# Optimization experiments

Measured on AMD Instinct MI355X. Metric: run time of the kernel, lower is better.

## Reference

```python
import jax, jax.numpy as jnp
import numpy as np

USER_NUM = 100000
ITEM_NUM = 100000
EMB = 128
N_USERS = 65536
N_BEH = 2097152
N_GROUPS = 2048


def setup_inputs() -> dict:
    key = jax.random.key(0)
    ks = jax.random.split(key, 7)
    user_ids = jax.random.randint(ks[0], (N_USERS,), 0, USER_NUM, dtype=jnp.int32)
    user_group_ids = jnp.sort(jax.random.randint(ks[1], (N_USERS,), 0, N_GROUPS, dtype=jnp.int32))
    behavior_item_ids = jax.random.randint(ks[2], (N_BEH,), 0, ITEM_NUM, dtype=jnp.int32)
    behavior_counts = jax.random.uniform(ks[3], (N_BEH,), dtype=jnp.float32)
    behavior_user_ids = jnp.sort(jax.random.randint(ks[4], (N_BEH,), 0, N_USERS, dtype=jnp.int32))
    user_table = jax.random.normal(ks[5], (USER_NUM, EMB), dtype=jnp.float32)
    item_table = jax.random.normal(ks[6], (ITEM_NUM, EMB), dtype=jnp.float32)
    return {
        "user_ids": user_ids,
        "user_group_ids": user_group_ids,
        "behavior_item_ids": behavior_item_ids,
        "behavior_counts": behavior_counts,
        "behavior_user_ids": behavior_user_ids,
        "user_table": user_table,
        "item_table": item_table,
        "num_groups": N_GROUPS,
    }


def reference(user_ids, user_group_ids, behavior_item_ids, behavior_counts,
              behavior_user_ids, user_table, item_table, num_groups):
    n_users = user_ids.shape[0]
    # weighted bag-of-items per user: sum_j item_emb[b_id] * count  -> [n_users, EMB]
    beh_emb = item_table[behavior_item_ids] * behavior_counts[:, None]
    per_user_beh = jax.ops.segment_sum(beh_emb, behavior_user_ids, num_segments=n_users)
    # user embedding with padding_idx=0 (id 0 -> zero vector)
    ue = user_table[user_ids] * (user_ids != 0).astype(user_table.dtype)[:, None]
    per_user = per_user_beh * ue  # personalized behavior embedding
    # pooling == 'sum' over users within each group -> [num_groups, EMB]
    group_embedding = jax.ops.segment_sum(per_user, user_group_ids, num_segments=num_groups)
    return group_embedding
```

## Files before the change

kernel.cpp:

```cpp
#include <hip/hip_runtime.h>
#include <hip/hip_fp16.h>

#define EMB 128

__global__ __launch_bounds__(256) void convert_kernel(
    const float* __restrict__ src, __half* __restrict__ dst, int n8)
{
    int t = blockIdx.x * 256 + threadIdx.x;
    if (t >= n8) return;
    const float4* s = (const float4*)src + (size_t)t * 2;
    float4 f0 = s[0];
    float4 f1 = s[1];
    union { __half h[8]; uint4 u; } pk;
    pk.h[0] = __float2half_rn(f0.x); pk.h[1] = __float2half_rn(f0.y);
    pk.h[2] = __float2half_rn(f0.z); pk.h[3] = __float2half_rn(f0.w);
    pk.h[4] = __float2half_rn(f1.x); pk.h[5] = __float2half_rn(f1.y);
    pk.h[6] = __float2half_rn(f1.z); pk.h[7] = __float2half_rn(f1.w);
    ((uint4*)dst)[t] = pk.u;
}

__global__ __launch_bounds__(256) void boundary_kernel(
    const int* __restrict__ beh_user, int* __restrict__ start,
    int n_beh, int n_users)
{
    int j = blockIdx.x * 256 + threadIdx.x;
    if (j >= n_beh) return;
    int cur  = beh_user[j];
    int prev = (j == 0) ? -1 : beh_user[j - 1];
    if (cur != prev) {
        for (int u = prev + 1; u <= cur; ++u) start[u] = j;
    }
    if (j == n_beh - 1) {
        for (int u = cur + 1; u <= n_users; ++u) start[u] = n_beh;
    }
}

__global__ __launch_bounds__(256) void per_user_kernel(
    const int*    __restrict__ user_ids,
    const int*    __restrict__ group_ids,
    const int*    __restrict__ beh_item,
    const float*  __restrict__ beh_cnt,
    const int*    __restrict__ beh_user,
    const float*  __restrict__ user_table,
    const __half* __restrict__ item_f16,
    const int*    __restrict__ start,
    float*        __restrict__ out,
    int n_users, int n_beh)
{
    const int lane = threadIdx.x & 63;
    const int half = lane >> 5;
    const int sub  = lane & 31;
    const int wave = threadIdx.x >> 6;
    const int user = blockIdx.x * 4 + wave;

    __shared__ float lds_acc[EMB];
    __shared__ int   lds_grp[4];
    if (threadIdx.x < EMB) lds_acc[threadIdx.x] = 0.0f;

    float4 acc = make_float4(0.f, 0.f, 0.f, 0.f);
    int g = -1;

    if (user < n_users) {
        int s, e;
        if (start) {
            s = start[user];
            e = start[user + 1];
        } else {
            int lo = 0, hi = n_beh;
            while (lo < hi) { int m = (lo + hi) >> 1; if (beh_user[m] < user) lo = m + 1; else hi = m; }
            s = lo;
            hi = n_beh;
            while (lo < hi) { int m = (lo + hi) >> 1; if (beh_user[m] <= user) lo = m + 1; else hi = m; }
            e = lo;
        }

        const __half* itp = item_f16 + sub * 4;

        int j = s;
        for (; j + 16 <= e; j += 16) {
            const int base = j + half * 8;
            int   bidx[8];
            float bcnt[8];
            #pragma unroll
            for (int k = 0; k < 8; ++k) { bidx[k] = beh_item[base + k]; bcnt[k] = beh_cnt[base + k]; }
            uint2 raw[8];
            #pragma unroll
            for (int k = 0; k < 8; ++k)
                raw[k] = *(const uint2*)(itp + (size_t)bidx[k] * EMB);
            #pragma unroll
            for (int k = 0; k < 8; ++k) {
                float2 f01 = __half22float2(*(const __half2*)&raw[k].x);
                float2 f23 = __half22float2(*(const __half2*)&raw[k].y);
                float  c   = bcnt[k];
                acc.x = fmaf(f01.x, c, acc.x);
                acc.y = fmaf(f01.y, c, acc.y);
                acc.z = fmaf(f23.x, c, acc.z);
                acc.w = fmaf(f23.y, c, acc.w);
            }
        }
        for (; j < e; j += 2) {
            int   jj = j + half;
            int   bi = 0;
            float c  = 0.f;
            if (jj < e) { bi = beh_item[jj]; c = beh_cnt[jj]; }
            uint2 raw = *(const uint2*)(itp + (size_t)bi * EMB);
            float2 f01 = __half22float2(*(const __half2*)&raw.x);
            float2 f23 = __half22float2(*(const __half2*)&raw.y);
            acc.x = fmaf(f01.x, c, acc.x);
            acc.y = fmaf(f01.y, c, acc.y);
            acc.z = fmaf(f23.x, c, acc.z);
            acc.w = fmaf(f23.y, c, acc.w);
        }

        acc.x += __shfl_xor(acc.x, 32, 64);
        acc.y += __shfl_xor(acc.y, 32, 64);
        acc.z += __shfl_xor(acc.z, 32, 64);
        acc.w += __shfl_xor(acc.w, 32, 64);

        int uid = user_ids[user];
        float4 ue = make_float4(0.f, 0.f, 0.f, 0.f);
        if (uid != 0) ue = *(const float4*)(user_table + (size_t)uid * EMB + sub * 4);
        acc.x *= ue.x; acc.y *= ue.y; acc.z *= ue.z; acc.w *= ue.w;

        g = group_ids[user];
    }

    const int   d0 = sub * 4 + half * 2;
    const float v0 = half ? acc.z : acc.x;
    const float v1 = half ? acc.w : acc.y;

    if (lane == 0) lds_grp[wave] = g;
    __syncthreads();

    int g0 = lds_grp[0];
    bool same = (g0 >= 0) && (lds_grp[1] == g0) && (lds_grp[2] == g0) && (lds_grp[3] == g0);
    if (same) {
        atomicAdd(&lds_acc[d0],     v0);
        atomicAdd(&lds_acc[d0 + 1], v1);
        __syncthreads();
        if (wave == 0) {
            atomicAdd(&out[(size_t)g0 * EMB + d0],     lds_acc[d0]);
            atomicAdd(&out[(size_t)g0 * EMB + d0 + 1], lds_acc[d0 + 1]);
        }
    } else if (g >= 0) {
        atomicAdd(&out[(size_t)g * EMB + d0],     v0);
        atomicAdd(&out[(size_t)g * EMB + d0 + 1], v1);
    }
}

__global__ __launch_bounds__(256) void per_user_f32_kernel(
    const int*   __restrict__ user_ids,
    const int*   __restrict__ group_ids,
    const int*   __restrict__ beh_item,
    const float* __restrict__ beh_cnt,
    const int*   __restrict__ beh_user,
    const float* __restrict__ user_table,
    const float* __restrict__ item_f32,
    float*       __restrict__ out,
    int n_users, int n_beh)
{
    const int lane = threadIdx.x & 63;
    const int wave = threadIdx.x >> 6;
    const int user = blockIdx.x * 4 + wave;
    float2 acc = make_float2(0.f, 0.f);
    int g = -1;
    if (user < n_users) {
        int lo = 0, hi = n_beh;
        while (lo < hi) { int m = (lo + hi) >> 1; if (beh_user[m] < user) lo = m + 1; else hi = m; }
        int s = lo; hi = n_beh;
        while (lo < hi) { int m = (lo + hi) >> 1; if (beh_user[m] <= user) lo = m + 1; else hi = m; }
        int e = lo;
        for (int j = s; j < e; ++j) {
            int   b = beh_item[j];
            float c = beh_cnt[j];
            float2 v = *(const float2*)(item_f32 + (size_t)b * EMB + lane * 2);
            acc.x = fmaf(v.x, c, acc.x);
            acc.y = fmaf(v.y, c, acc.y);
        }
        int uid = user_ids[user];
        float2 ue = make_float2(0.f, 0.f);
        if (uid != 0) ue = *(const float2*)(user_table + (size_t)uid * EMB + lane * 2);
        acc.x *= ue.x; acc.y *= ue.y;
        g = group_ids[user];
    }
    if (g >= 0) {
        atomicAdd(&out[(size_t)g * EMB + lane * 2],     acc.x);
        atomicAdd(&out[(size_t)g * EMB + lane * 2 + 1], acc.y);
    }
}

extern "C" void kernel_launch(void* const* d_in, const int* in_sizes, int n_in,
                              void* d_out, int out_size, void* d_ws, size_t ws_size,
                              hipStream_t stream) {
    const int*   user_ids   = (const int*)  d_in[0];
    const int*   group_ids  = (const int*)  d_in[1];
    const int*   beh_item   = (const int*)  d_in[2];
    const float* beh_cnt    = (const float*)d_in[3];
    const int*   beh_user   = (const int*)  d_in[4];
    const float* user_table = (const float*)d_in[5];
    const float* item_table = (const float*)d_in[6];

    const int n_users = in_sizes[0];
    const int n_beh   = in_sizes[2];
    const int item_n  = in_sizes[6] / EMB;

    float* out = (float*)d_out;
    hipMemsetAsync(out, 0, (size_t)out_size * sizeof(float), stream);

    size_t start_bytes = (size_t)(n_users + 1) * sizeof(int);
    size_t f16_off     = (start_bytes + 255) & ~(size_t)255;
    size_t f16_bytes   = (size_t)item_n * EMB * sizeof(__half);

    if (ws_size < f16_off + f16_bytes) {
        int ublocks = (n_users + 3) / 4;
        per_user_f32_kernel<<<ublocks, 256, 0, stream>>>(
            user_ids, group_ids, beh_item, beh_cnt, beh_user,
            user_table, item_table, out, n_users, n_beh);
        return;
    }

    int*    start    = (int*)d_ws;
    __half* item_f16 = (__half*)((char*)d_ws + f16_off);

    boundary_kernel<<<(n_beh + 255) / 256, 256, 0, stream>>>(beh_user, start, n_beh, n_users);

    int n8 = (item_n * EMB) / 8;
    convert_kernel<<<(n8 + 255) / 256, 256, 0, stream>>>(item_table, item_f16, n8);

    int ublocks = (n_users + 3) / 4;
    per_user_kernel<<<ublocks, 256, 0, stream>>>(
        user_ids, group_ids, beh_item, beh_cnt, beh_user,
        user_table, item_f16, start, out, n_users, n_beh);
}
```

Baseline: 244.9 us.

## Fuse prep kernels and gather items with 16-byte loads, prefetched indices

Merges the fp16 conversion and segment-boundary kernels into one launch to save a launch and a dependency. The per-user gather now has 16 lanes cover one 128-wide fp16 row with 16-byte loads, so each wave processes four behaviors per step. Behavior indices and counts are loaded cooperatively, one per lane, then broadcast with shuffles, and the next batch is prefetched a step ahead. The cost is a second cross-lane reduction stage, more accumulator registers, and masked-out lanes in the tail batch.

```diff
diff --git a/kernel.cpp b/kernel.cpp
--- a/kernel.cpp
+++ b/kernel.cpp
@@ -3,53 +3,61 @@
 
 #define EMB 128
 
-__global__ __launch_bounds__(256) void convert_kernel(
-    const float* __restrict__ src, __half* __restrict__ dst, int n8)
-{
-    int t = blockIdx.x * 256 + threadIdx.x;
-    if (t >= n8) return;
-    const float4* s = (const float4*)src + (size_t)t * 2;
-    float4 f0 = s[0];
-    float4 f1 = s[1];
-    union { __half h[8]; uint4 u; } pk;
-    pk.h[0] = __float2half_rn(f0.x); pk.h[1] = __float2half_rn(f0.y);
-    pk.h[2] = __float2half_rn(f0.z); pk.h[3] = __float2half_rn(f0.w);
-    pk.h[4] = __float2half_rn(f1.x); pk.h[5] = __float2half_rn(f1.y);
-    pk.h[6] = __float2half_rn(f1.z); pk.h[7] = __float2half_rn(f1.w);
-    ((uint4*)dst)[t] = pk.u;
-}
-
-__global__ __launch_bounds__(256) void boundary_kernel(
+__global__ __launch_bounds__(256) void prep_kernel(
+    const float* __restrict__ src, __half* __restrict__ dst, int n8,
     const int* __restrict__ beh_user, int* __restrict__ start,
     int n_beh, int n_users)
 {
-    int j = blockIdx.x * 256 + threadIdx.x;
-    if (j >= n_beh) return;
-    int cur  = beh_user[j];
-    int prev = (j == 0) ? -1 : beh_user[j - 1];
-    if (cur != prev) {
-        for (int u = prev + 1; u <= cur; ++u) start[u] = j;
-    }
-    if (j == n_beh - 1) {
-        for (int u = cur + 1; u <= n_users; ++u) start[u] = n_beh;
-    }
-}
+    int t = blockIdx.x * 256 + threadIdx.x;
+    if (t < n8) {
+        const float4* s = (const float4*)src + (size_t)t * 2;
+        float4 f0 = s[0];
+        float4 f1 = s[1];
+        union { __half h[8]; uint4 u; } pk;
+        pk.h[0] = __float2half_rn(f0.x); pk.h[1] = __float2half_rn(f0.y);
+        pk.h[2] = __float2half_rn(f0.z); pk.h[3] = __float2half_rn(f0.w);
+        pk.h[4] = __float2half_rn(f1.x); pk.h[5] = __float2half_rn(f1.y);
+        pk.h[6] = __float2half_rn(f1.z); pk.h[7] = __float2half_rn(f1.w);
+        ((uint4*)dst)[t] = pk.u;
+    }
+    if (t < n_beh) {
+        int cur  = beh_user[t];
+        int prev = (t == 0) ? -1 : beh_user[t - 1];
+        if (cur != prev) {
+            for (int u = prev + 1; u <= cur; ++u) start[u] = t;
+        }
+        if (t == n_beh - 1) {
+            for (int u = cur + 1; u <= n_users; ++u) start[u] = n_beh;
+        }
+    }
+}
+
+#define ACCUM(W_, c)                                              \
+    {                                                             \
+        float2 f01 = __half22float2(*(const __half2*)&(W_).x);    \
+        float2 f23 = __half22float2(*(const __half2*)&(W_).y);    \
+        float2 f45 = __half22float2(*(const __half2*)&(W_).z);    \
+        float2 f67 = __half22float2(*(const __half2*)&(W_).w);    \
+        a0 = fmaf(f01.x, (c), a0); a1 = fmaf(f01.y, (c), a1);     \
+        a2 = fmaf(f23.x, (c), a2); a3 = fmaf(f23.y, (c), a3);     \
+        a4 = fmaf(f45.x, (c), a4); a5 = fmaf(f45.y, (c), a5);     \
+        a6 = fmaf(f67.x, (c), a6); a7 = fmaf(f67.y, (c), a7);     \
+    }
 
 __global__ __launch_bounds__(256) void per_user_kernel(
     const int*    __restrict__ user_ids,
     const int*    __restrict__ group_ids,
     const int*    __restrict__ beh_item,
     const float*  __restrict__ beh_cnt,
-    const int*    __restrict__ beh_user,
     const float*  __restrict__ user_table,
     const __half* __restrict__ item_f16,
     const int*    __restrict__ start,
     float*        __restrict__ out,
-    int n_users, int n_beh)
+    int n_users)
 {
     const int lane = threadIdx.x & 63;
-    const int half = lane >> 5;
-    const int sub  = lane & 31;
+    const int q    = lane >> 4;
+    const int r    = lane & 15;
     const int wave = threadIdx.x >> 6;
     const int user = blockIdx.x * 4 + wave;
 
@@ -57,90 +65,96 @@
     __shared__ int   lds_grp[4];
     if (threadIdx.x < EMB) lds_acc[threadIdx.x] = 0.0f;
 
-    float4 acc = make_float4(0.f, 0.f, 0.f, 0.f);
+    float a0 = 0.f, a1 = 0.f, a2 = 0.f, a3 = 0.f;
+    float a4 = 0.f, a5 = 0.f, a6 = 0.f, a7 = 0.f;
     int g = -1;
 
     if (user < n_users) {
-        int s, e;
-        if (start) {
-            s = start[user];
-            e = start[user + 1];
+        const int s = start[user];
+        const int e = start[user + 1];
+
+        const __half* itp = item_f16 + r * 8;
+
+        int   idx_c = 0;
+        float cnt_c = 0.f;
+        {
+            int t0 = s + r;
+            if (t0 < e) { idx_c = beh_item[t0]; cnt_c = beh_cnt[t0]; }
+        }
+
+        for (int j = s; j < e; j += 16) {
+            int   idx_n = 0;
+            float cnt_n = 0.f;
+            int   tn = j + 16 + r;
+            if (tn < e) { idx_n = beh_item[tn]; cnt_n = beh_cnt[tn]; }
+
+            int   bi0 = __shfl(idx_c, q * 4 + 0, 16);
+            int   bi1 = __shfl(idx_c, q * 4 + 1, 16);
+            int   bi2 = __shfl(idx_c, q * 4 + 2, 16);
+            int   bi3 = __shfl(idx_c, q * 4 + 3, 16);
+            float c0  = __shfl(cnt_c, q * 4 + 0, 16);
+            float c1  = __shfl(cnt_c, q * 4 + 1, 16);
+            float c2  = __shfl(cnt_c, q * 4 + 2, 16);
+            float c3  = __shfl(cnt_c, q * 4 + 3, 16);
+
+            uint4 w0 = *(const uint4*)(itp + (size_t)bi0 * EMB);
+            uint4 w1 = *(const uint4*)(itp + (size_t)bi1 * EMB);
+            uint4 w2 = *(const uint4*)(itp + (size_t)bi2 * EMB);
+            uint4 w3 = *(const uint4*)(itp + (size_t)bi3 * EMB);
+
+            ACCUM(w0, c0);
+            ACCUM(w1, c1);
+            ACCUM(w2, c2);
+            ACCUM(w3, c3);
+
+            idx_c = idx_n;
+            cnt_c = cnt_n;
+        }
+
+        a0 += __shfl_xor(a0, 16, 64); a1 += __shfl_xor(a1, 16, 64);
+        a2 += __shfl_xor(a2, 16, 64); a3 += __shfl_xor(a3, 16, 64);
+        a4 += __shfl_xor(a4, 16, 64); a5 += __shfl_xor(a5, 16, 64);
+        a6 += __shfl_xor(a6, 16, 64); a7 += __shfl_xor(a7, 16, 64);
+        a0 += __shfl_xor(a0, 32, 64); a1 += __shfl_xor(a1, 32, 64);
+        a2 += __shfl_xor(a2, 32, 64); a3 += __shfl_xor(a3, 32, 64);
+        a4 += __shfl_xor(a4, 32, 64); a5 += __shfl_xor(a5, 32, 64);
+        a6 += __shfl_xor(a6, 32, 64); a7 += __shfl_xor(a7, 32, 64);
+
+        const int uid = user_ids[user];
+        if (uid != 0) {
+            const float* up = user_table + (size_t)uid * EMB + r * 8;
+            float4 u0 = *(const float4*)up;
+            float4 u1 = *(const float4*)(up + 4);
+            a0 *= u0.x; a1 *= u0.y; a2 *= u0.z; a3 *= u0.w;
+            a4 *= u1.x; a5 *= u1.y; a6 *= u1.z; a7 *= u1.w;
         } else {
-            int lo = 0, hi = n_beh;
-            while (lo < hi) { int m = (lo + hi) >> 1; if (beh_user[m] < user) lo = m + 1; else hi = m; }
-            s = lo;
-            hi = n_beh;
-            while (lo < hi) { int m = (lo + hi) >> 1; if (beh_user[m] <= user) lo = m + 1; else hi = m; }
-            e = lo;
-        }
-
-        const __half* itp = item_f16 + sub * 4;
-
-        int j = s;
-        for (; j + 16 <= e; j += 16) {
-            const int base = j + half * 8;
-            int   bidx[8];
-            float bcnt[8];
-            #pragma unroll
-            for (int k = 0; k < 8; ++k) { bidx[k] = beh_item[base + k]; bcnt[k] = beh_cnt[base + k]; }
-            uint2 raw[8];
-            #pragma unroll
-            for (int k = 0; k < 8; ++k)
-                raw[k] = *(const uint2*)(itp + (size_t)bidx[k] * EMB);
-            #pragma unroll
-            for (int k = 0; k < 8; ++k) {
-                float2 f01 = __half22float2(*(const __half2*)&raw[k].x);
-                float2 f23 = __half22float2(*(const __half2*)&raw[k].y);
-                float  c   = bcnt[k];
-                acc.x = fmaf(f01.x, c, acc.x);
-                acc.y = fmaf(f01.y, c, acc.y);
-                acc.z = fmaf(f23.x, c, acc.z);
-                acc.w = fmaf(f23.y, c, acc.w);
-            }
-        }
-        for (; j < e; j += 2) {
-            int   jj = j + half;
-            int   bi = 0;
-            float c  = 0.f;
-            if (jj < e) { bi = beh_item[jj]; c = beh_cnt[jj]; }
-            uint2 raw = *(const uint2*)(itp + (size_t)bi * EMB);
-            float2 f01 = __half22float2(*(const __half2*)&raw.x);
-            float2 f23 = __half22float2(*(const __half2*)&raw.y);
-            acc.x = fmaf(f01.x, c, acc.x);
-            acc.y = fmaf(f01.y, c, acc.y);
-            acc.z = fmaf(f23.x, c, acc.z);
-            acc.w = fmaf(f23.y, c, acc.w);
-        }
-
-        acc.x += __shfl_xor(acc.x, 32, 64);
-        acc.y += __shfl_xor(acc.y, 32, 64);
-        acc.z += __shfl_xor(acc.z, 32, 64);
-        acc.w += __shfl_xor(acc.w, 32, 64);
-
-        int uid = user_ids[user];
-        float4 ue = make_float4(0.f, 0.f, 0.f, 0.f);
-        if (uid != 0) ue = *(const float4*)(user_table + (size_t)uid * EMB + sub * 4);
-        acc.x *= ue.x; acc.y *= ue.y; acc.z *= ue.z; acc.w *= ue.w;
+            a0 = a1 = a2 = a3 = a4 = a5 = a6 = a7 = 0.f;
+        }
 
         g = group_ids[user];
     }
 
-    const int   d0 = sub * 4 + half * 2;
-    const float v0 = half ? acc.z : acc.x;
-    const float v1 = half ? acc.w : acc.y;
+    float v0, v1;
+    if      (q == 0) { v0 = a0; v1 = a1; }
+    else if (q == 1) { v0 = a2; v1 = a3; }
+    else if (q == 2) { v0 = a4; v1 = a5; }
+    else             { v0 = a6; v1 = a7; }
+    const int d0 = r * 8 + q * 2;
 
     if (lane == 0) lds_grp[wave] = g;
     __syncthreads();
 
-    int g0 = lds_grp[0];
-    bool same = (g0 >= 0) && (lds_grp[1] == g0) && (lds_grp[2] == g0) && (lds_grp[3] == g0);
+    const int g0 = lds_grp[0];
+    const bool same = (g0 >= 0) && (lds_grp[1] == g0) &&
+                      (lds_grp[2] == g0) && (lds_grp[3] == g0);
     if (same) {
         atomicAdd(&lds_acc[d0],     v0);
         atomicAdd(&lds_acc[d0 + 1], v1);
         __syncthreads();
-        if (wave == 0) {
-            atomicAdd(&out[(size_t)g0 * EMB + d0],     lds_acc[d0]);
-            atomicAdd(&out[(size_t)g0 * EMB + d0 + 1], lds_acc[d0 + 1]);
+        if (threadIdx.x < 64) {
+            const int d = threadIdx.x * 2;
+            atomicAdd(&out[(size_t)g0 * EMB + d],     lds_acc[d]);
+            atomicAdd(&out[(size_t)g0 * EMB + d + 1], lds_acc[d + 1]);
         }
     } else if (g >= 0) {
         atomicAdd(&out[(size_t)g * EMB + d0],     v0);
@@ -205,7 +219,7 @@
     const int item_n  = in_sizes[6] / EMB;
 
     float* out = (float*)d_out;
-    hipMemsetAsync(out, 0, (size_t)out_size * sizeof(float), stream);
+    (void)hipMemsetAsync(out, 0, (size_t)out_size * sizeof(float), stream);
 
     size_t start_bytes = (size_t)(n_users + 1) * sizeof(int);
     size_t f16_off     = (start_bytes + 255) & ~(size_t)255;
@@ -222,13 +236,13 @@
     int*    start    = (int*)d_ws;
     __half* item_f16 = (__half*)((char*)d_ws + f16_off);
 
-    boundary_kernel<<<(n_beh + 255) / 256, 256, 0, stream>>>(beh_user, start, n_beh, n_users);
-
     int n8 = (item_n * EMB) / 8;
-    convert_kernel<<<(n8 + 255) / 256, 256, 0, stream>>>(item_table, item_f16, n8);
+    int prep_n = n8 > n_beh ? n8 : n_beh;
+    prep_kernel<<<(prep_n + 255) / 256, 256, 0, stream>>>(
+        item_table, item_f16, n8, beh_user, start, n_beh, n_users);
 
     int ublocks = (n_users + 3) / 4;
     per_user_kernel<<<ublocks, 256, 0, stream>>>(
-        user_ids, group_ids, beh_item, beh_cnt, beh_user,
-        user_table, item_f16, start, out, n_users, n_beh);
-}
+        user_ids, group_ids, beh_item, beh_cnt,
+        user_table, item_f16, start, out, n_users);
+}
```

New measurement: 233.0 us. 4.9% less time.
